# Optimization experiments

Hardware: AMD Instinct MI355X
Metric: run time of the kernel (lower is better)

## Reference

```python
import jax, jax.numpy as jnp
import numpy as np

B, D, NQ, NS = 64, 64, 2048, 2048

def setup_inputs() -> dict:
    key = jax.random.key(0)
    k1, k2 = jax.random.split(key)
    query_local = jax.random.normal(k1, (B, D, NQ), dtype=jnp.float32)
    support_local = jax.random.normal(k2, (B, D, NS), dtype=jnp.float32)
    return {"query_local": query_local, "support_local": support_local}

def reference(query_local, support_local):
    # sim[b, q, s] = sum_d query[b, d, q] * support[b, d, s]  -> (B, N_q, N_s)
    sim = jnp.einsum('bdq,bds->bqs', query_local, support_local)
    best_sim = jnp.max(sim, axis=2)        # (B, N_q)
    return jnp.mean(best_sim, axis=1)      # (B,)
```

## Files before the change

kernel.cpp:

```cpp
#include <hip/hip_runtime.h>
#include <hip/hip_bf16.h>

#define NB 64
#define ND 64
#define NQ 2048
#define NS 2048
#define QBLK 256
#define SBLK 64
#define QPB 8
#define NSPLIT 4
#define NSS (NS / NSPLIT)
#define NT (NSS / SBLK)

typedef float f32x4 __attribute__((ext_vector_type(4)));
typedef short bf16x8 __attribute__((ext_vector_type(8)));
typedef int i32x4 __attribute__((ext_vector_type(4)));

__device__ inline i32x4 pack8(const float* f) {
  union { __hip_bfloat162 h2[4]; i32x4 v; } u;
  #pragma unroll
  for (int p = 0; p < 4; ++p)
    u.h2[p] = __float22bfloat162_rn(float2{f[2 * p], f[2 * p + 1]});
  return u.v;
}

__global__ __launch_bounds__(256, 4) void bmd_main(
    const float* __restrict__ Q, const float* __restrict__ S,
    float* __restrict__ part) {
  const int bid = blockIdx.x;
  const int b  = bid & (NB - 1);
  const int qb = (bid >> 6) & (QPB - 1);
  const int ss = bid >> 9;
  const int q0 = qb * QBLK;
  const int sbase = ss * NSS;
  const int tid = threadIdx.x;
  const int lane = tid & 63;
  const int w = tid >> 6;

  __shared__ char sT[2][SBLK * 128];

  const float* Qb = Q + (size_t)b * ND * NQ;
  const float* Sb = S + (size_t)b * ND * NS;

  i32x4 afrag[4][2];
  {
    const int qrow = q0 + w * 64 + (lane & 15);
    const int dbase = (lane >> 4) * 8;
    for (int mf = 0; mf < 4; ++mf)
      for (int ks = 0; ks < 2; ++ks) {
        const int d0 = ks * 32 + dbase;
        float f[8];
        #pragma unroll
        for (int e = 0; e < 8; ++e)
          f[e] = Qb[(size_t)(d0 + e) * NQ + (qrow + mf * 16)];
        afrag[mf][ks] = pack8(f);
      }
  }

  f32x4 rmax[4];
  #pragma unroll
  for (int mf = 0; mf < 4; ++mf)
    rmax[mf] = f32x4{-INFINITY, -INFINITY, -INFINITY, -INFINITY};

  const int dbq = (tid >> 3) & 7;
  const int sl0 = (tid & 7) + (w << 3);
  const float* stage_src = Sb + (size_t)dbq * 8 * NS + sbase;
  int sl[2], byt[2];
  #pragma unroll
  for (int i = 0; i < 2; ++i) {
    sl[i] = sl0 + i * 32;
    byt[i] = sl[i] * 128 + ((dbq ^ (sl[i] & 7)) << 4);
  }

  #pragma unroll
  for (int i = 0; i < 2; ++i) {
    const float* src = stage_src + sl[i];
    float f[8];
    #pragma unroll
    for (int e = 0; e < 8; ++e) f[e] = src[(size_t)e * NS];
    *reinterpret_cast<i32x4*>(sT[0] + byt[i]) = pack8(f);
  }
  __syncthreads();

  int cur = 0;
  for (int t = 0; t < NT; ++t) {
    float pf[2][8];
    const bool has_next = (t + 1 < NT);
    if (has_next) {
      const float* src = stage_src + (t + 1) * SBLK;
      #pragma unroll
      for (int i = 0; i < 2; ++i)
        #pragma unroll
        for (int e = 0; e < 8; ++e)
          pf[i][e] = src[sl[i] + (size_t)e * NS];
    }

    #pragma unroll
    for (int nfp = 0; nfp < 2; ++nfp) {
      const int scol0 = nfp * 32 + (lane & 15);
      bf16x8 bfr0[2], bfr1[2];
      #pragma unroll
      for (int ks = 0; ks < 2; ++ks) {
        const int slot = ((ks * 4 + (lane >> 4)) ^ (scol0 & 7)) << 4;
        bfr0[ks] = *reinterpret_cast<const bf16x8*>(sT[cur] + scol0 * 128 + slot);
        bfr1[ks] = *reinterpret_cast<const bf16x8*>(sT[cur] + (scol0 + 16) * 128 + slot);
      }
      #pragma unroll
      for (int mf = 0; mf < 4; ++mf) {
        const bf16x8 a0 = __builtin_bit_cast(bf16x8, afrag[mf][0]);
        const bf16x8 a1 = __builtin_bit_cast(bf16x8, afrag[mf][1]);
        f32x4 acc0 = {0.f, 0.f, 0.f, 0.f};
        f32x4 acc1 = {0.f, 0.f, 0.f, 0.f};
        acc0 = __builtin_amdgcn_mfma_f32_16x16x32_bf16(a0, bfr0[0], acc0, 0, 0, 0);
        acc1 = __builtin_amdgcn_mfma_f32_16x16x32_bf16(a0, bfr1[0], acc1, 0, 0, 0);
        acc0 = __builtin_amdgcn_mfma_f32_16x16x32_bf16(a1, bfr0[1], acc0, 0, 0, 0);
        acc1 = __builtin_amdgcn_mfma_f32_16x16x32_bf16(a1, bfr1[1], acc1, 0, 0, 0);
        #pragma unroll
        for (int j = 0; j < 4; ++j)
          rmax[mf][j] = fmaxf(rmax[mf][j], fmaxf(acc0[j], acc1[j]));
      }
    }

    if (has_next) {
      #pragma unroll
      for (int i = 0; i < 2; ++i)
        *reinterpret_cast<i32x4*>(sT[cur ^ 1] + byt[i]) = pack8(pf[i]);
    }
    __syncthreads();
    cur ^= 1;
  }

  float* rowp = part + (size_t)bid * QBLK + w * 64;
  #pragma unroll
  for (int mf = 0; mf < 4; ++mf) {
    #pragma unroll
    for (int j = 0; j < 4; ++j) {
      float v = rmax[mf][j];
      v = fmaxf(v, __shfl_xor(v, 1));
      v = fmaxf(v, __shfl_xor(v, 2));
      v = fmaxf(v, __shfl_xor(v, 4));
      v = fmaxf(v, __shfl_xor(v, 8));
      if ((lane & 15) == 0)
        rowp[mf * 16 + (lane >> 4) * 4 + j] = v;
    }
  }
}

__global__ void bmd_reduce(const float* __restrict__ part, float* __restrict__ out) {
  const int b = blockIdx.x;
  const int tid = threadIdx.x;
  __shared__ float ws4[4];
  float sum = 0.f;
  for (int qb = 0; qb < QPB; ++qb) {
    float m = -INFINITY;
    #pragma unroll
    for (int ssi = 0; ssi < NSPLIT; ++ssi)
      m = fmaxf(m, part[((size_t)((ssi * QPB + qb) * NB + b)) * QBLK + tid]);
    sum += m;
  }
  #pragma unroll
  for (int o = 1; o < 64; o <<= 1) sum += __shfl_xor(sum, o);
  if ((tid & 63) == 0) ws4[tid >> 6] = sum;
  __syncthreads();
  if (tid == 0) out[b] = (ws4[0] + ws4[1] + ws4[2] + ws4[3]) * (1.0f / NQ);
}

extern "C" void kernel_launch(void* const* d_in, const int* in_sizes, int n_in,
                              void* d_out, int out_size, void* d_ws, size_t ws_size,
                              hipStream_t stream) {
  const float* Q = (const float*)d_in[0];
  const float* S = (const float*)d_in[1];
  float* out = (float*)d_out;
  float* part = (float*)d_ws;
  bmd_main<<<dim3(NB * QPB * NSPLIT), dim3(256), 0, stream>>>(Q, S, part);
  bmd_reduce<<<dim3(NB), dim3(256), 0, stream>>>(part, out);
}
```

Baseline: 51.13 us.

## Double query tile per block to 512 rows with 512 threads sharing support tile

Each block now covers 512 query rows with 8 waves instead of 256 rows with 4 waves, so every staged support tile in LDS feeds twice as many MFMAs. Each thread now loads one support chunk per step instead of two, halving redundant global reads and bf16 conversion of support. The grid shrinks to 1024 blocks, and the reduce kernel is re-indexed for the new partial layout. Larger blocks with launch bounds of 512 threads may limit register budget and occupancy.

```diff
diff --git a/kernel.cpp b/kernel.cpp
--- a/kernel.cpp
+++ b/kernel.cpp
@@ -5,9 +5,9 @@
 #define ND 64
 #define NQ 2048
 #define NS 2048
-#define QBLK 256
+#define QBLK 512
 #define SBLK 64
-#define QPB 8
+#define QPB 4
 #define NSPLIT 4
 #define NSS (NS / NSPLIT)
 #define NT (NSS / SBLK)
@@ -24,13 +24,13 @@
   return u.v;
 }
 
-__global__ __launch_bounds__(256, 4) void bmd_main(
+__global__ __launch_bounds__(512, 4) void bmd_main(
     const float* __restrict__ Q, const float* __restrict__ S,
     float* __restrict__ part) {
   const int bid = blockIdx.x;
   const int b  = bid & (NB - 1);
   const int qb = (bid >> 6) & (QPB - 1);
-  const int ss = bid >> 9;
+  const int ss = bid >> 8;
   const int q0 = qb * QBLK;
   const int sbase = ss * NSS;
   const int tid = threadIdx.x;
@@ -57,42 +57,34 @@
       }
   }
 
+  const f32x4 kZero = {0.f, 0.f, 0.f, 0.f};
   f32x4 rmax[4];
   #pragma unroll
   for (int mf = 0; mf < 4; ++mf)
     rmax[mf] = f32x4{-INFINITY, -INFINITY, -INFINITY, -INFINITY};
 
   const int dbq = (tid >> 3) & 7;
-  const int sl0 = (tid & 7) + (w << 3);
+  const int sl = (tid & 7) + ((tid >> 6) << 3);
+  const int byt = sl * 128 + ((dbq ^ (sl & 7)) << 4);
   const float* stage_src = Sb + (size_t)dbq * 8 * NS + sbase;
-  int sl[2], byt[2];
-  #pragma unroll
-  for (int i = 0; i < 2; ++i) {
-    sl[i] = sl0 + i * 32;
-    byt[i] = sl[i] * 128 + ((dbq ^ (sl[i] & 7)) << 4);
-  }
 
-  #pragma unroll
-  for (int i = 0; i < 2; ++i) {
-    const float* src = stage_src + sl[i];
+  {
+    const float* src = stage_src + sl;
     float f[8];
     #pragma unroll
     for (int e = 0; e < 8; ++e) f[e] = src[(size_t)e * NS];
-    *reinterpret_cast<i32x4*>(sT[0] + byt[i]) = pack8(f);
+    *reinterpret_cast<i32x4*>(sT[0] + byt) = pack8(f);
   }
   __syncthreads();
 
   int cur = 0;
   for (int t = 0; t < NT; ++t) {
-    float pf[2][8];
+    float pf[8];
     const bool has_next = (t + 1 < NT);
     if (has_next) {
-      const float* src = stage_src + (t + 1) * SBLK;
+      const float* src = stage_src + (t + 1) * SBLK + sl;
       #pragma unroll
-      for (int i = 0; i < 2; ++i)
-        #pragma unroll
-        for (int e = 0; e < 8; ++e)
-          pf[i][e] = src[sl[i] + (size_t)e * NS];
+      for (int e = 0; e < 8; ++e) pf[e] = src[(size_t)e * NS];
     }
 
     #pragma unroll
@@ -109,10 +101,8 @@
       for (int mf = 0; mf < 4; ++mf) {
         const bf16x8 a0 = __builtin_bit_cast(bf16x8, afrag[mf][0]);
         const bf16x8 a1 = __builtin_bit_cast(bf16x8, afrag[mf][1]);
-        f32x4 acc0 = {0.f, 0.f, 0.f, 0.f};
-        f32x4 acc1 = {0.f, 0.f, 0.f, 0.f};
-        acc0 = __builtin_amdgcn_mfma_f32_16x16x32_bf16(a0, bfr0[0], acc0, 0, 0, 0);
-        acc1 = __builtin_amdgcn_mfma_f32_16x16x32_bf16(a0, bfr1[0], acc1, 0, 0, 0);
+        f32x4 acc0 = __builtin_amdgcn_mfma_f32_16x16x32_bf16(a0, bfr0[0], kZero, 0, 0, 0);
+        f32x4 acc1 = __builtin_amdgcn_mfma_f32_16x16x32_bf16(a0, bfr1[0], kZero, 0, 0, 0);
         acc0 = __builtin_amdgcn_mfma_f32_16x16x32_bf16(a1, bfr0[1], acc0, 0, 0, 0);
         acc1 = __builtin_amdgcn_mfma_f32_16x16x32_bf16(a1, bfr1[1], acc1, 0, 0, 0);
         #pragma unroll
@@ -121,11 +111,8 @@
       }
     }
 
-    if (has_next) {
-      #pragma unroll
-      for (int i = 0; i < 2; ++i)
-        *reinterpret_cast<i32x4*>(sT[cur ^ 1] + byt[i]) = pack8(pf[i]);
-    }
+    if (has_next)
+      *reinterpret_cast<i32x4*>(sT[cur ^ 1] + byt) = pack8(pf);
     __syncthreads();
     cur ^= 1;
   }
@@ -151,11 +138,15 @@
   const int tid = threadIdx.x;
   __shared__ float ws4[4];
   float sum = 0.f;
-  for (int qb = 0; qb < QPB; ++qb) {
+  #pragma unroll
+  for (int k = 0; k < NQ / 256; ++k) {
+    const int q = k * 256 + tid;
+    const int qb = q >> 9;
+    const int row = q & (QBLK - 1);
     float m = -INFINITY;
     #pragma unroll
     for (int ssi = 0; ssi < NSPLIT; ++ssi)
-      m = fmaxf(m, part[((size_t)((ssi * QPB + qb) * NB + b)) * QBLK + tid]);
+      m = fmaxf(m, part[((size_t)((ssi * QPB + qb) * NB + b)) * QBLK + row]);
     sum += m;
   }
   #pragma unroll
@@ -172,6 +163,6 @@
   const float* S = (const float*)d_in[1];
   float* out = (float*)d_out;
   float* part = (float*)d_ws;
-  bmd_main<<<dim3(NB * QPB * NSPLIT), dim3(256), 0, stream>>>(Q, S, part);
+  bmd_main<<<dim3(NB * QPB * NSPLIT), dim3(512), 0, stream>>>(Q, S, part);
   bmd_reduce<<<dim3(NB), dim3(256), 0, stream>>>(part, out);
 }
```

After: 49.05 us. 1.04x faster.
